# Performance work log

Measured on AMD Instinct MI355X. Metric: run time of the kernel, lower is better.

The kernel has to match this reference:

```python
import jax, jax.numpy as jnp
import numpy as np

N = 100000
E = 1600000
F_IN = 256
F_OUT = 128
ALPHA = 0.2  # leaky relu slope


def setup_inputs() -> dict:
    key = jax.random.key(0)
    ks = jax.random.split(key, 8)
    x = jax.random.normal(ks[0], (N, F_IN), dtype=jnp.float32)
    edge_index = jax.random.randint(ks[1], (2, E), 0, N, dtype=jnp.int64)
    edge_attr = jax.random.normal(ks[2], (E,), dtype=jnp.float32)
    # xavier-normal-ish params
    weight = jax.random.normal(ks[3], (F_IN, F_OUT), dtype=jnp.float32) * (1.414 * np.sqrt(2.0 / (F_IN + F_OUT)))
    bias = jnp.zeros((F_OUT,), dtype=jnp.float32)
    a_l = jax.random.normal(ks[4], (F_OUT,), dtype=jnp.float32) * 0.1
    a_r = jax.random.normal(ks[5], (F_OUT,), dtype=jnp.float32) * 0.1
    fc = jax.random.normal(ks[6], (F_OUT, 1), dtype=jnp.float32) * (1.414 * np.sqrt(2.0 / (F_OUT + 1)))
    bf = jnp.zeros((1,), dtype=jnp.float32)
    return {"x": x, "edge_index": edge_index, "edge_attr": edge_attr,
            "weight": weight, "bias": bias, "a_l": a_l, "a_r": a_r,
            "fc": fc, "bf": bf}


def _segment_softmax(val, seg, num_segments):
    # numerically stable softmax over edges grouped by destination row
    seg_max = jax.ops.segment_max(val, seg, num_segments=num_segments)
    val = jnp.exp(val - seg_max[seg])
    seg_sum = jax.ops.segment_sum(val, seg, num_segments=num_segments)
    return val / (seg_sum[seg] + 1e-16)


def reference(x, edge_index, edge_attr, weight, bias, a_l, a_r, fc, bf):
    # dropout layers are identity in eval mode (deterministic reference)
    h = x @ weight                                   # [N, F_OUT]
    row, col = edge_index[0], edge_index[1]          # dst, src
    # GAT-style edge attention: leaky_relu(a_l.h[dst] + a_r.h[src])
    score_l = h @ a_l                                # [N]
    score_r = h @ a_r                                # [N]
    e = score_l[row] + score_r[col]                  # [E]
    e = jnp.where(e > 0, e, ALPHA * e)
    # row-softmax normalization over incoming edges of each dst node
    val = _segment_softmax(e, row, N)                # [E]
    # spmm: out[i] = sum_{(i,j) in E} val_ij * h[j]
    val_h = jax.ops.segment_sum(val[:, None] * h[col], row, num_segments=N)  # [N, F_OUT]
    val_h = jnp.where(jnp.isnan(val_h), 0.0, val_h)
    val_h = val_h + bias
    # NodeAdaptiveEncoder: relu(x) + sigmoid(x@fc + bf) * min(x, 0)
    gate = jax.nn.sigmoid(val_h @ fc + bf)           # [N, 1]
    out = jnp.where(val_h < 0, 0.0, val_h) + gate * jnp.where(val_h > 0, 0.0, val_h)
    return out
```

## Files before the change

kernel.cpp:

```cpp
#include <hip/hip_runtime.h>

#define N_NODES 100000
#define N_EDGES 1600000
#define FIN 256
#define FOUT 128
#define LRELU_ALPHA 0.2f

#define NBUCKET 391
#define PBLOCKS 256
#define PCHUNK  (N_EDGES / PBLOCKS)
#define BCAP    5120

using bf16x8 = __attribute__((ext_vector_type(8))) short;
using f32x4  = __attribute__((ext_vector_type(4))) float;

static __device__ __forceinline__ unsigned short f2bf(float f) {
    union { float f; unsigned u; } v; v.f = f;
    unsigned r = (v.u + 0x7FFF + ((v.u >> 16) & 1)) >> 16;
    return (unsigned short)r;
}

static __device__ __forceinline__ bf16x8 cvt8(float4 a, float4 b) {
    union { bf16x8 v; unsigned short u[8]; } r;
    r.u[0] = f2bf(a.x); r.u[1] = f2bf(a.y); r.u[2] = f2bf(a.z); r.u[3] = f2bf(a.w);
    r.u[4] = f2bf(b.x); r.u[5] = f2bf(b.y); r.u[6] = f2bf(b.z); r.u[7] = f2bf(b.w);
    return r.v;
}

static __device__ __forceinline__ void gld_lds16(const unsigned short* g, unsigned short* l) {
    __builtin_amdgcn_global_load_lds(
        (const __attribute__((address_space(1))) unsigned int*)g,
        (__attribute__((address_space(3))) unsigned int*)l, 16, 0, 0);
}

__global__ void k_wt(const float* __restrict__ w, unsigned short* __restrict__ wt_sw)
{
    int i = blockIdx.x * blockDim.x + threadIdx.x;
    if (i >= FIN * FOUT) return;
    int k = i >> 7, n = i & 127;
    wt_sw[n * FIN + (((k >> 3) ^ (n & 7)) << 3) + (k & 7)] = f2bf(w[k * FOUT + n]);
}

__global__ __launch_bounds__(256, 2) void k_gemm3(
    const float* __restrict__ x, const unsigned short* __restrict__ wt_sw,
    const float* __restrict__ a_l, const float* __restrict__ a_r,
    unsigned short* __restrict__ hb, float* __restrict__ score_l,
    float* __restrict__ score_r)
{
    __shared__ unsigned short wlds[FOUT * FIN];

    const int tid  = threadIdx.x;
    const int lane = tid & 63;
    const int wid  = tid >> 6;
    const int m    = lane & 15;
    const int q    = lane >> 4;

    {
        const unsigned short* g = wt_sw + wid * 8192;
        unsigned short*       l = wlds  + wid * 8192;
#pragma unroll
        for (int i = 0; i < 16; ++i)
            gld_lds16(g + i * 512 + lane * 8, l + i * 512);
    }

    const int row0 = blockIdx.x * 128 + wid * 32;
    int r0 = row0 + m;       if (r0 > N_NODES - 1) r0 = N_NODES - 1;
    int r1 = row0 + 16 + m;  if (r1 > N_NODES - 1) r1 = N_NODES - 1;
    const float* xp0 = x + (long)r0 * FIN + q * 8;
    const float* xp1 = x + (long)r1 * FIN + q * 8;

    float4 xb[2][2][2];
    xb[0][0][0] = *(const float4*)(xp0);        xb[0][0][1] = *(const float4*)(xp0 + 4);
    xb[0][1][0] = *(const float4*)(xp1);        xb[0][1][1] = *(const float4*)(xp1 + 4);
    xb[1][0][0] = *(const float4*)(xp0 + 32);   xb[1][0][1] = *(const float4*)(xp0 + 36);
    xb[1][1][0] = *(const float4*)(xp1 + 32);   xb[1][1][1] = *(const float4*)(xp1 + 36);

    f32x4 acc[2][8];
#pragma unroll
    for (int mt = 0; mt < 2; ++mt)
#pragma unroll
        for (int nt = 0; nt < 8; ++nt) acc[mt][nt] = (f32x4){0.f, 0.f, 0.f, 0.f};

    __syncthreads();

    const int xr = m & 7;

    bf16x8 bfr[2][8];
#pragma unroll
    for (int nt = 0; nt < 8; ++nt)
        bfr[0][nt] = *(const bf16x8*)&wlds[(nt * 16 + m) * FIN + ((q ^ xr) << 3)];

#pragma unroll
    for (int s = 0; s < 8; ++s) {
        const int p = s & 1;
        bf16x8 a0 = cvt8(xb[p][0][0], xb[p][0][1]);
        bf16x8 a1 = cvt8(xb[p][1][0], xb[p][1][1]);
        if (s + 2 < 8) {
            xb[p][0][0] = *(const float4*)(xp0 + (s + 2) * 32);
            xb[p][0][1] = *(const float4*)(xp0 + (s + 2) * 32 + 4);
            xb[p][1][0] = *(const float4*)(xp1 + (s + 2) * 32);
            xb[p][1][1] = *(const float4*)(xp1 + (s + 2) * 32 + 4);
        }
        if (s + 1 < 8) {
#pragma unroll
            for (int nt = 0; nt < 8; ++nt)
                bfr[1 - p][nt] = *(const bf16x8*)
                    &wlds[(nt * 16 + m) * FIN + ((((s + 1) * 4 + q) ^ xr) << 3)];
        }
#pragma unroll
        for (int nt = 0; nt < 8; ++nt) {
            acc[0][nt] = __builtin_amdgcn_mfma_f32_16x16x32_bf16(a0, bfr[p][nt], acc[0][nt], 0, 0, 0);
            acc[1][nt] = __builtin_amdgcn_mfma_f32_16x16x32_bf16(a1, bfr[p][nt], acc[1][nt], 0, 0, 0);
        }
    }

    float al[8], ar[8];
#pragma unroll
    for (int nt = 0; nt < 8; ++nt) { al[nt] = a_l[nt * 16 + m]; ar[nt] = a_r[nt * 16 + m]; }

#pragma unroll
    for (int mt = 0; mt < 2; ++mt) {
#pragma unroll
        for (int r = 0; r < 4; ++r) {
            const int node = row0 + mt * 16 + q * 4 + r;
            const bool ok = node < N_NODES;
            float sl = 0.f, sr = 0.f;
#pragma unroll
            for (int nt = 0; nt < 8; ++nt) {
                float v = acc[mt][nt][r];
                if (ok) hb[node * FOUT + nt * 16 + m] = f2bf(v);
                sl = fmaf(v, al[nt], sl);
                sr = fmaf(v, ar[nt], sr);
            }
#pragma unroll
            for (int msk = 1; msk < 16; msk <<= 1) {
                sl += __shfl_xor(sl, msk, 64);
                sr += __shfl_xor(sr, msk, 64);
            }
            if (ok && m == 0) { score_l[node] = sl; score_r[node] = sr; }
        }
    }
}

__global__ __launch_bounds__(256) void k_bhist(const int* __restrict__ ei,
                                               int* __restrict__ bcnt)
{
    __shared__ int c[NBUCKET];
    for (int i = threadIdx.x; i < NBUCKET; i += 256) c[i] = 0;
    __syncthreads();
    int i = blockIdx.x * 256 + threadIdx.x;
    if (i < N_EDGES / 2) {
        int2 rr = ((const int2*)ei)[i];
        atomicAdd(&c[rr.x >> 8], 1);
        atomicAdd(&c[rr.y >> 8], 1);
    }
    __syncthreads();
    for (int i2 = threadIdx.x; i2 < NBUCKET; i2 += 256)
        if (c[i2]) atomicAdd(&bcnt[i2], c[i2]);
}

__global__ __launch_bounds__(512) void k_bscan(const int* __restrict__ bcnt,
                                               int* __restrict__ bbase,
                                               int* __restrict__ gcur,
                                               int* __restrict__ rowptr)
{
    __shared__ int s[512];
    const int tid = threadIdx.x;
    int v = (tid < NBUCKET) ? bcnt[tid] : 0;
    s[tid] = v;
    __syncthreads();
    for (int off = 1; off < 512; off <<= 1) {
        int t = (tid >= off) ? s[tid - off] : 0;
        __syncthreads();
        s[tid] += t;
        __syncthreads();
    }
    if (tid < NBUCKET) {
        int excl = s[tid] - v;
        bbase[tid] = excl;
        gcur[tid]  = excl;
    }
    if (tid == NBUCKET - 1) bbase[NBUCKET] = s[tid];
    if (tid == 0) rowptr[N_NODES] = N_EDGES;
}

__global__ __launch_bounds__(512) void k_part(const int* __restrict__ ei,
                                              int* __restrict__ gcur,
                                              unsigned* __restrict__ part)
{
    __shared__ unsigned staging[PCHUNK];
    __shared__ unsigned short bkt[PCHUNK];
    __shared__ int cnt[512];
    __shared__ int loc[512];
    __shared__ int gbase[NBUCKET];

    const int tid = threadIdx.x;
    const int e0  = blockIdx.x * PCHUNK;

    cnt[tid] = 0;
    __syncthreads();

    for (int i = tid; i < PCHUNK; i += 512)
        atomicAdd(&cnt[ei[e0 + i] >> 8], 1);
    __syncthreads();

    int v = cnt[tid];
    loc[tid] = v;
    __syncthreads();
    for (int off = 1; off < 512; off <<= 1) {
        int t = (tid >= off) ? loc[tid - off] : 0;
        __syncthreads();
        loc[tid] += t;
        __syncthreads();
    }
    int excl = loc[tid] - v;
    if (tid < NBUCKET && v > 0) gbase[tid] = atomicAdd(&gcur[tid], v);
    loc[tid] = excl;
    cnt[tid] = excl;
    __syncthreads();

    for (int i = tid; i < PCHUNK; i += 512) {
        int dst = ei[e0 + i];
        int src = ei[N_EDGES + e0 + i];
        int b = dst >> 8;
        unsigned rec = ((unsigned)(dst & 255) << 17) | (unsigned)src;
        int p = atomicAdd(&cnt[b], 1);
        staging[p] = rec;
        bkt[p] = (unsigned short)b;
    }
    __syncthreads();

    for (int i = tid; i < PCHUNK; i += 512) {
        int b = bkt[i];
        part[gbase[b] + (i - loc[b])] = staging[i];
    }
}

__global__ __launch_bounds__(512) void k_bucket(const unsigned* __restrict__ part,
                                                const int* __restrict__ bbase,
                                                int* __restrict__ rowptr,
                                                unsigned* __restrict__ csrs)
{
    __shared__ unsigned rin[BCAP];
    __shared__ unsigned rs[BCAP];
    __shared__ int hist[256];
    __shared__ int tmp[512];

    const int b   = blockIdx.x;
    const int tid = threadIdx.x;
    const int beg = bbase[b];
    int cnt = bbase[b + 1] - beg;
    if (cnt > BCAP) cnt = BCAP;
    const int d0 = b << 8;

    if (tid < 256) hist[tid] = 0;
    __syncthreads();

    for (int i = tid; i < cnt; i += 512) {
        unsigned rec = part[beg + i];
        rin[i] = rec;
        atomicAdd(&hist[rec >> 17], 1);
    }
    __syncthreads();

    int v = (tid < 256) ? hist[tid] : 0;
    tmp[tid] = v;
    __syncthreads();
    for (int off = 1; off < 512; off <<= 1) {
        int t = (tid >= off) ? tmp[tid - off] : 0;
        __syncthreads();
        tmp[tid] += t;
        __syncthreads();
    }
    if (tid < 256) {
        int excl = tmp[tid] - v;
        hist[tid] = excl;
        int d = d0 + tid;
        if (d < N_NODES) rowptr[d] = beg + excl;
    }
    __syncthreads();

    for (int i = tid; i < cnt; i += 512) {
        unsigned rec = rin[i];
        int p = atomicAdd(&hist[rec >> 17], 1);
        rs[p] = rec;
    }
    __syncthreads();

    for (int i = tid; i < cnt; i += 512)
        csrs[beg + i] = rs[i];
}

__global__ __launch_bounds__(256) void k_spmm_gate(
    const int* __restrict__ rowptr, const unsigned* __restrict__ csrs,
    const unsigned short* __restrict__ hb,
    const float* __restrict__ score_l, const float* __restrict__ score_r,
    const float* __restrict__ bias, const float* __restrict__ fc,
    const float* __restrict__ bf, float* __restrict__ out)
{
    const int lane = threadIdx.x & 63;
    const int slot = lane >> 4;
    const int t    = lane & 15;
    const int node = blockIdx.x * 4 + (threadIdx.x >> 6);
    if (node >= N_NODES) return;

    const int beg = rowptr[node], end = rowptr[node + 1];
    const float sl = score_l[node];

    float acc[8];
#pragma unroll
    for (int i = 0; i < 8; ++i) acc[i] = 0.f;
    float denom = 0.f;

    for (int j = beg + slot; j < end; j += 8) {
        int  j1  = j + 4;
        bool h2  = j1 < end;
        int s0 = csrs[j] & 0x1FFFF;
        int s1 = h2 ? (csrs[j1] & 0x1FFFF) : 0;
        float e0 = sl + score_r[s0];
        float e1 = sl + score_r[s1];
        e0 = e0 > 0.f ? e0 : LRELU_ALPHA * e0;
        e1 = e1 > 0.f ? e1 : LRELU_ALPHA * e1;
        float w0 = __expf(e0);
        float w1 = h2 ? __expf(e1) : 0.f;
        int4 g0 = *(const int4*)&hb[s0 * FOUT + t * 8];
        int4 g1 = *(const int4*)&hb[s1 * FOUT + t * 8];
        denom += w0 + w1;
        acc[0] = fmaf(w0, __int_as_float(g0.x << 16),         acc[0]);
        acc[1] = fmaf(w0, __int_as_float(g0.x & 0xFFFF0000),  acc[1]);
        acc[2] = fmaf(w0, __int_as_float(g0.y << 16),         acc[2]);
        acc[3] = fmaf(w0, __int_as_float(g0.y & 0xFFFF0000),  acc[3]);
        acc[4] = fmaf(w0, __int_as_float(g0.z << 16),         acc[4]);
        acc[5] = fmaf(w0, __int_as_float(g0.z & 0xFFFF0000),  acc[5]);
        acc[6] = fmaf(w0, __int_as_float(g0.w << 16),         acc[6]);
        acc[7] = fmaf(w0, __int_as_float(g0.w & 0xFFFF0000),  acc[7]);
        acc[0] = fmaf(w1, __int_as_float(g1.x << 16),         acc[0]);
        acc[1] = fmaf(w1, __int_as_float(g1.x & 0xFFFF0000),  acc[1]);
        acc[2] = fmaf(w1, __int_as_float(g1.y << 16),         acc[2]);
        acc[3] = fmaf(w1, __int_as_float(g1.y & 0xFFFF0000),  acc[3]);
        acc[4] = fmaf(w1, __int_as_float(g1.z << 16),         acc[4]);
        acc[5] = fmaf(w1, __int_as_float(g1.z & 0xFFFF0000),  acc[5]);
        acc[6] = fmaf(w1, __int_as_float(g1.w << 16),         acc[6]);
        acc[7] = fmaf(w1, __int_as_float(g1.w & 0xFFFF0000),  acc[7]);
    }

#pragma unroll
    for (int i = 0; i < 8; ++i) {
        acc[i] += __shfl_xor(acc[i], 16, 64);
        acc[i] += __shfl_xor(acc[i], 32, 64);
    }
    denom += __shfl_xor(denom, 16, 64);
    denom += __shfl_xor(denom, 32, 64);

    float inv = 1.0f / (denom + 1e-16f);

    float vx[8], part = 0.f;
#pragma unroll
    for (int i = 0; i < 8; ++i) {
        vx[i] = fmaf(acc[i], inv, bias[t * 8 + i]);
        part = fmaf(vx[i], fc[t * 8 + i], part);
    }
#pragma unroll
    for (int msk = 1; msk < 16; msk <<= 1) part += __shfl_xor(part, msk, 64);
    float g = 1.0f / (1.0f + __expf(-(part + bf[0])));

    if (slot == 0) {
        float4 o0, o1;
        float* ov0 = &o0.x; float* ov1 = &o1.x;
#pragma unroll
        for (int i = 0; i < 4; ++i) {
            float v2 = vx[i];
            ov0[i] = (v2 < 0.f ? 0.f : v2) + g * (v2 > 0.f ? 0.f : v2);
        }
#pragma unroll
        for (int i = 0; i < 4; ++i) {
            float v2 = vx[4 + i];
            ov1[i] = (v2 < 0.f ? 0.f : v2) + g * (v2 > 0.f ? 0.f : v2);
        }
        *(float4*)&out[node * FOUT + t * 8]     = o0;
        *(float4*)&out[node * FOUT + t * 8 + 4] = o1;
    }
}

extern "C" void kernel_launch(void* const* d_in, const int* in_sizes, int n_in,
                              void* d_out, int out_size, void* d_ws, size_t ws_size,
                              hipStream_t stream)
{
    const float* x      = (const float*)d_in[0];
    const int*   ei     = (const int*)d_in[1];
    const float* weight = (const float*)d_in[3];
    const float* bias   = (const float*)d_in[4];
    const float* a_l    = (const float*)d_in[5];
    const float* a_r    = (const float*)d_in[6];
    const float* fc     = (const float*)d_in[7];
    const float* bf     = (const float*)d_in[8];
    float* out = (float*)d_out;

    char* ws = (char*)d_ws;
    unsigned short* hb      = (unsigned short*)(ws);
    unsigned short* wt_sw   = (unsigned short*)(ws + 25600000);
    float*          score_l = (float*)(ws + 25665536);
    float*          score_r = (float*)(ws + 26065536);
    int*            bcnt    = (int*)  (ws + 26465536);
    int*            bbase   = (int*)  (ws + 26467584);
    int*            gcur    = (int*)  (ws + 26469632);
    int*            rowptr  = (int*)  (ws + 26471680);
    unsigned*       part    = (unsigned*)(ws + 26871744);
    unsigned*       csrs    = (unsigned*)(ws + 33271744);

    hipMemsetAsync(bcnt, 0, NBUCKET * sizeof(int), stream);

    k_wt<<<(FIN * FOUT + 255) / 256, 256, 0, stream>>>(weight, wt_sw);

    k_gemm3<<<(N_NODES + 127) / 128, 256, 0, stream>>>(
        x, wt_sw, a_l, a_r, hb, score_l, score_r);

    k_bhist<<<(N_EDGES / 2 + 255) / 256, 256, 0, stream>>>(ei, bcnt);
    k_bscan<<<1, 512, 0, stream>>>(bcnt, bbase, gcur, rowptr);
    k_part<<<PBLOCKS, 512, 0, stream>>>(ei, gcur, part);
    k_bucket<<<NBUCKET, 512, 0, stream>>>(part, bbase, rowptr, csrs);

    k_spmm_gate<<<(N_NODES + 3) / 4, 256, 0, stream>>>(
        rowptr, csrs, hb, score_l, score_r, bias, fc, bf, out);
}
```

Measured before the change: 356.7 us.

## Use fixed-capacity bucket slots, drop histogram/scan kernels, one node per 16 lanes

Removes the bucket histogram and scan kernels by giving each destination bucket a fixed BCAP-sized slot in the partition buffer, with the bucket counter zeroed inside k_wt instead of by a memset. CSR rows are now described by separate begin/end arrays. The SpMM kernel assigns one node per 16 lanes instead of one per 64-lane wave, which drops the cross-slot shuffles, and uses packed 2-wide float math for the bf16 accumulation. The cost is that any bucket holding more than BCAP edges silently drops edges, and each node's neighbours are now walked serially by one 16-lane group.

```diff
diff --git a/kernel.cpp b/kernel.cpp
--- a/kernel.cpp
+++ b/kernel.cpp
@@ -13,6 +13,7 @@
 
 using bf16x8 = __attribute__((ext_vector_type(8))) short;
 using f32x4  = __attribute__((ext_vector_type(4))) float;
+using v2f    = __attribute__((ext_vector_type(2))) float;
 
 static __device__ __forceinline__ unsigned short f2bf(float f) {
     union { float f; unsigned u; } v; v.f = f;
@@ -33,8 +34,18 @@
         (__attribute__((address_space(3))) unsigned int*)l, 16, 0, 0);
 }
 
-__global__ void k_wt(const float* __restrict__ w, unsigned short* __restrict__ wt_sw)
-{
+static __device__ __forceinline__ v2f up2(unsigned u) {
+    v2f r;
+    r.x = __int_as_float((int)(u << 16));
+    r.y = __int_as_float((int)(u & 0xFFFF0000u));
+    return r;
+}
+
+__global__ void k_wt(const float* __restrict__ w, unsigned short* __restrict__ wt_sw,
+                     int* __restrict__ bcnt)
+{
+    if (blockIdx.x == 0)
+        for (int z = threadIdx.x; z < NBUCKET; z += 256) bcnt[z] = 0;
     int i = blockIdx.x * blockDim.x + threadIdx.x;
     if (i >= FIN * FOUT) return;
     int k = i >> 7, n = i & 127;
@@ -142,50 +153,8 @@
     }
 }
 
-__global__ __launch_bounds__(256) void k_bhist(const int* __restrict__ ei,
-                                               int* __restrict__ bcnt)
-{
-    __shared__ int c[NBUCKET];
-    for (int i = threadIdx.x; i < NBUCKET; i += 256) c[i] = 0;
-    __syncthreads();
-    int i = blockIdx.x * 256 + threadIdx.x;
-    if (i < N_EDGES / 2) {
-        int2 rr = ((const int2*)ei)[i];
-        atomicAdd(&c[rr.x >> 8], 1);
-        atomicAdd(&c[rr.y >> 8], 1);
-    }
-    __syncthreads();
-    for (int i2 = threadIdx.x; i2 < NBUCKET; i2 += 256)
-        if (c[i2]) atomicAdd(&bcnt[i2], c[i2]);
-}
-
-__global__ __launch_bounds__(512) void k_bscan(const int* __restrict__ bcnt,
-                                               int* __restrict__ bbase,
-                                               int* __restrict__ gcur,
-                                               int* __restrict__ rowptr)
-{
-    __shared__ int s[512];
-    const int tid = threadIdx.x;
-    int v = (tid < NBUCKET) ? bcnt[tid] : 0;
-    s[tid] = v;
-    __syncthreads();
-    for (int off = 1; off < 512; off <<= 1) {
-        int t = (tid >= off) ? s[tid - off] : 0;
-        __syncthreads();
-        s[tid] += t;
-        __syncthreads();
-    }
-    if (tid < NBUCKET) {
-        int excl = s[tid] - v;
-        bbase[tid] = excl;
-        gcur[tid]  = excl;
-    }
-    if (tid == NBUCKET - 1) bbase[NBUCKET] = s[tid];
-    if (tid == 0) rowptr[N_NODES] = N_EDGES;
-}
-
 __global__ __launch_bounds__(512) void k_part(const int* __restrict__ ei,
-                                              int* __restrict__ gcur,
+                                              int* __restrict__ bcnt,
                                               unsigned* __restrict__ part)
 {
     __shared__ unsigned staging[PCHUNK];
@@ -214,7 +183,7 @@
         __syncthreads();
     }
     int excl = loc[tid] - v;
-    if (tid < NBUCKET && v > 0) gbase[tid] = atomicAdd(&gcur[tid], v);
+    if (tid < NBUCKET && v > 0) gbase[tid] = atomicAdd(&bcnt[tid], v);
     loc[tid] = excl;
     cnt[tid] = excl;
     __syncthreads();
@@ -232,13 +201,15 @@
 
     for (int i = tid; i < PCHUNK; i += 512) {
         int b = bkt[i];
-        part[gbase[b] + (i - loc[b])] = staging[i];
+        int off = gbase[b] + (i - loc[b]);
+        if (off < BCAP) part[b * BCAP + off] = staging[i];
     }
 }
 
 __global__ __launch_bounds__(512) void k_bucket(const unsigned* __restrict__ part,
-                                                const int* __restrict__ bbase,
-                                                int* __restrict__ rowptr,
+                                                const int* __restrict__ bcnt,
+                                                int* __restrict__ rowbeg,
+                                                int* __restrict__ rowend,
                                                 unsigned* __restrict__ csrs)
 {
     __shared__ unsigned rin[BCAP];
@@ -248,8 +219,8 @@
 
     const int b   = blockIdx.x;
     const int tid = threadIdx.x;
-    const int beg = bbase[b];
-    int cnt = bbase[b + 1] - beg;
+    const int beg = b * BCAP;
+    int cnt = bcnt[b];
     if (cnt > BCAP) cnt = BCAP;
     const int d0 = b << 8;
 
@@ -276,7 +247,7 @@
         int excl = tmp[tid] - v;
         hist[tid] = excl;
         int d = d0 + tid;
-        if (d < N_NODES) rowptr[d] = beg + excl;
+        if (d < N_NODES) { rowbeg[d] = beg + excl; rowend[d] = beg + excl + v; }
     }
     __syncthreads();
 
@@ -292,94 +263,75 @@
 }
 
 __global__ __launch_bounds__(256) void k_spmm_gate(
-    const int* __restrict__ rowptr, const unsigned* __restrict__ csrs,
+    const int* __restrict__ rowbeg, const int* __restrict__ rowend,
+    const unsigned* __restrict__ csrs,
     const unsigned short* __restrict__ hb,
     const float* __restrict__ score_l, const float* __restrict__ score_r,
     const float* __restrict__ bias, const float* __restrict__ fc,
     const float* __restrict__ bf, float* __restrict__ out)
 {
-    const int lane = threadIdx.x & 63;
-    const int slot = lane >> 4;
-    const int t    = lane & 15;
-    const int node = blockIdx.x * 4 + (threadIdx.x >> 6);
+    const int t    = threadIdx.x & 15;
+    const int node = blockIdx.x * 16 + (threadIdx.x >> 4);
     if (node >= N_NODES) return;
 
-    const int beg = rowptr[node], end = rowptr[node + 1];
+    const int beg = rowbeg[node], end = rowend[node];
     const float sl = score_l[node];
 
-    float acc[8];
-#pragma unroll
-    for (int i = 0; i < 8; ++i) acc[i] = 0.f;
+    v2f acc0 = {0.f, 0.f}, acc1 = {0.f, 0.f}, acc2 = {0.f, 0.f}, acc3 = {0.f, 0.f};
     float denom = 0.f;
 
-    for (int j = beg + slot; j < end; j += 8) {
-        int  j1  = j + 4;
-        bool h2  = j1 < end;
-        int s0 = csrs[j] & 0x1FFFF;
-        int s1 = h2 ? (csrs[j1] & 0x1FFFF) : 0;
+    for (int j = beg; j < end; j += 2) {
+        bool h2 = (j + 1) < end;
+        unsigned r0 = csrs[j];
+        unsigned r1 = h2 ? csrs[j + 1] : r0;
+        int s0 = r0 & 0x1FFFF;
+        int s1 = r1 & 0x1FFFF;
         float e0 = sl + score_r[s0];
         float e1 = sl + score_r[s1];
         e0 = e0 > 0.f ? e0 : LRELU_ALPHA * e0;
         e1 = e1 > 0.f ? e1 : LRELU_ALPHA * e1;
         float w0 = __expf(e0);
         float w1 = h2 ? __expf(e1) : 0.f;
-        int4 g0 = *(const int4*)&hb[s0 * FOUT + t * 8];
-        int4 g1 = *(const int4*)&hb[s1 * FOUT + t * 8];
+        uint4 g0 = *(const uint4*)&hb[s0 * FOUT + t * 8];
+        uint4 g1 = *(const uint4*)&hb[s1 * FOUT + t * 8];
         denom += w0 + w1;
-        acc[0] = fmaf(w0, __int_as_float(g0.x << 16),         acc[0]);
-        acc[1] = fmaf(w0, __int_as_float(g0.x & 0xFFFF0000),  acc[1]);
-        acc[2] = fmaf(w0, __int_as_float(g0.y << 16),         acc[2]);
-        acc[3] = fmaf(w0, __int_as_float(g0.y & 0xFFFF0000),  acc[3]);
-        acc[4] = fmaf(w0, __int_as_float(g0.z << 16),         acc[4]);
-        acc[5] = fmaf(w0, __int_as_float(g0.z & 0xFFFF0000),  acc[5]);
-        acc[6] = fmaf(w0, __int_as_float(g0.w << 16),         acc[6]);
-        acc[7] = fmaf(w0, __int_as_float(g0.w & 0xFFFF0000),  acc[7]);
-        acc[0] = fmaf(w1, __int_as_float(g1.x << 16),         acc[0]);
-        acc[1] = fmaf(w1, __int_as_float(g1.x & 0xFFFF0000),  acc[1]);
-        acc[2] = fmaf(w1, __int_as_float(g1.y << 16),         acc[2]);
-        acc[3] = fmaf(w1, __int_as_float(g1.y & 0xFFFF0000),  acc[3]);
-        acc[4] = fmaf(w1, __int_as_float(g1.z << 16),         acc[4]);
-        acc[5] = fmaf(w1, __int_as_float(g1.z & 0xFFFF0000),  acc[5]);
-        acc[6] = fmaf(w1, __int_as_float(g1.w << 16),         acc[6]);
-        acc[7] = fmaf(w1, __int_as_float(g1.w & 0xFFFF0000),  acc[7]);
-    }
-
+        v2f w02 = {w0, w0}, w12 = {w1, w1};
+        acc0 += w02 * up2(g0.x);  acc1 += w02 * up2(g0.y);
+        acc2 += w02 * up2(g0.z);  acc3 += w02 * up2(g0.w);
+        acc0 += w12 * up2(g1.x);  acc1 += w12 * up2(g1.y);
+        acc2 += w12 * up2(g1.z);  acc3 += w12 * up2(g1.w);
+    }
+
+    float inv = 1.0f / (denom + 1e-16f);
+
+    float vx[8];
+    vx[0] = acc0.x; vx[1] = acc0.y; vx[2] = acc1.x; vx[3] = acc1.y;
+    vx[4] = acc2.x; vx[5] = acc2.y; vx[6] = acc3.x; vx[7] = acc3.y;
+
+    float gp = 0.f;
 #pragma unroll
     for (int i = 0; i < 8; ++i) {
-        acc[i] += __shfl_xor(acc[i], 16, 64);
-        acc[i] += __shfl_xor(acc[i], 32, 64);
-    }
-    denom += __shfl_xor(denom, 16, 64);
-    denom += __shfl_xor(denom, 32, 64);
-
-    float inv = 1.0f / (denom + 1e-16f);
-
-    float vx[8], part = 0.f;
-#pragma unroll
-    for (int i = 0; i < 8; ++i) {
-        vx[i] = fmaf(acc[i], inv, bias[t * 8 + i]);
-        part = fmaf(vx[i], fc[t * 8 + i], part);
-    }
-#pragma unroll
-    for (int msk = 1; msk < 16; msk <<= 1) part += __shfl_xor(part, msk, 64);
-    float g = 1.0f / (1.0f + __expf(-(part + bf[0])));
-
-    if (slot == 0) {
-        float4 o0, o1;
-        float* ov0 = &o0.x; float* ov1 = &o1.x;
-#pragma unroll
-        for (int i = 0; i < 4; ++i) {
-            float v2 = vx[i];
-            ov0[i] = (v2 < 0.f ? 0.f : v2) + g * (v2 > 0.f ? 0.f : v2);
-        }
-#pragma unroll
-        for (int i = 0; i < 4; ++i) {
-            float v2 = vx[4 + i];
-            ov1[i] = (v2 < 0.f ? 0.f : v2) + g * (v2 > 0.f ? 0.f : v2);
-        }
-        *(float4*)&out[node * FOUT + t * 8]     = o0;
-        *(float4*)&out[node * FOUT + t * 8 + 4] = o1;
-    }
+        vx[i] = fmaf(vx[i], inv, bias[t * 8 + i]);
+        gp = fmaf(vx[i], fc[t * 8 + i], gp);
+    }
+#pragma unroll
+    for (int msk = 1; msk < 16; msk <<= 1) gp += __shfl_xor(gp, msk, 64);
+    float g = 1.0f / (1.0f + __expf(-(gp + bf[0])));
+
+    float4 o0, o1;
+    float* ov0 = &o0.x; float* ov1 = &o1.x;
+#pragma unroll
+    for (int i = 0; i < 4; ++i) {
+        float v2 = vx[i];
+        ov0[i] = (v2 < 0.f ? 0.f : v2) + g * (v2 > 0.f ? 0.f : v2);
+    }
+#pragma unroll
+    for (int i = 0; i < 4; ++i) {
+        float v2 = vx[4 + i];
+        ov1[i] = (v2 < 0.f ? 0.f : v2) + g * (v2 > 0.f ? 0.f : v2);
+    }
+    *(float4*)&out[node * FOUT + t * 8]     = o0;
+    *(float4*)&out[node * FOUT + t * 8 + 4] = o1;
 }
 
 extern "C" void kernel_launch(void* const* d_in, const int* in_sizes, int n_in,
@@ -402,24 +354,19 @@
     float*          score_l = (float*)(ws + 25665536);
     float*          score_r = (float*)(ws + 26065536);
     int*            bcnt    = (int*)  (ws + 26465536);
-    int*            bbase   = (int*)  (ws + 26467584);
-    int*            gcur    = (int*)  (ws + 26469632);
-    int*            rowptr  = (int*)  (ws + 26471680);
-    unsigned*       part    = (unsigned*)(ws + 26871744);
-    unsigned*       csrs    = (unsigned*)(ws + 33271744);
-
-    hipMemsetAsync(bcnt, 0, NBUCKET * sizeof(int), stream);
-
-    k_wt<<<(FIN * FOUT + 255) / 256, 256, 0, stream>>>(weight, wt_sw);
+    int*            rowbeg  = (int*)  (ws + 26467584);
+    int*            rowend  = (int*)  (ws + 26867584);
+    unsigned*       part    = (unsigned*)(ws + 27267584);
+    unsigned*       csrs    = (unsigned*)(ws + 35275264);
+
+    k_wt<<<(FIN * FOUT + 255) / 256, 256, 0, stream>>>(weight, wt_sw, bcnt);
 
     k_gemm3<<<(N_NODES + 127) / 128, 256, 0, stream>>>(
         x, wt_sw, a_l, a_r, hb, score_l, score_r);
 
-    k_bhist<<<(N_EDGES / 2 + 255) / 256, 256, 0, stream>>>(ei, bcnt);
-    k_bscan<<<1, 512, 0, stream>>>(bcnt, bbase, gcur, rowptr);
-    k_part<<<PBLOCKS, 512, 0, stream>>>(ei, gcur, part);
-    k_bucket<<<NBUCKET, 512, 0, stream>>>(part, bbase, rowptr, csrs);
-
-    k_spmm_gate<<<(N_NODES + 3) / 4, 256, 0, stream>>>(
-        rowptr, csrs, hb, score_l, score_r, bias, fc, bf, out);
-}
+    k_part<<<PBLOCKS, 512, 0, stream>>>(ei, bcnt, part);
+    k_bucket<<<NBUCKET, 512, 0, stream>>>(part, bcnt, rowbeg, rowend, csrs);
+
+    k_spmm_gate<<<(N_NODES + 15) / 16, 256, 0, stream>>>(
+        rowbeg, rowend, csrs, hb, score_l, score_r, bias, fc, bf, out);
+}
```

Result: faster. 295.9 us (-17.0%).
